# Kernel tuning notes

Hardware: AMD Instinct MI355X
Metric: run time of the kernel (lower is better)

Reference implementation:

```python
import jax, jax.numpy as jnp
import numpy as np

TEMPERATURE = 0.2
EPS = 1e-12

def _l2norm(x):
    # F.normalize(dim=1): x / max(||x||, eps)
    n = jnp.sqrt(jnp.sum(x * x, axis=1, keepdims=True))
    return x / jnp.maximum(n, EPS)

def setup_inputs() -> dict:
    key = jax.random.key(0)
    k1, k2, k3 = jax.random.split(key, 3)
    B, D, Q = 1024, 128, 65536
    return {
        "global_features_1": jax.random.normal(k1, (B, D), dtype=jnp.float32),
        "global_features_2": jax.random.normal(k2, (B, D), dtype=jnp.float32),
        "queue": jax.random.normal(k3, (Q, D), dtype=jnp.float32),
    }

def reference(global_features_1, global_features_2, queue):
    q = _l2norm(global_features_1)                    # [B, D]
    k = _l2norm(global_features_2)                    # [B, D]
    pos_sim = jnp.sum(q * k, axis=1, keepdims=True) / TEMPERATURE   # [B, 1]
    # queue renormalized under no_grad in the original
    queue_n = jax.lax.stop_gradient(_l2norm(queue))   # [Q, D]
    neg_sim = jnp.einsum('bd,qd->bq', q, queue_n) / TEMPERATURE     # [B, Q]
    logits = jnp.concatenate([pos_sim, neg_sim], axis=1)            # [B, 1+Q]
    # cross-entropy with label 0 for every row: -log_softmax(logits)[:, 0]
    log_probs = jax.nn.log_softmax(logits, axis=1)
    loss = -jnp.mean(log_probs[:, 0])
    return (loss, pos_sim, neg_sim)
```

## Files before the change

### kernel.cpp

```cpp
#include <hip/hip_runtime.h>
#include <math.h>

constexpr int B = 1024;
constexpr int D = 128;
constexpr int Q = 65536;
constexpr int NPART = 1024;
#define TEMP_INV 5.0f
#define EPS 1e-12f

typedef __bf16 bf16x8 __attribute__((ext_vector_type(8)));
typedef float  f32x4  __attribute__((ext_vector_type(4)));

__device__ __forceinline__ float wave_reduce_sum(float v) {
    #pragma unroll
    for (int off = 32; off > 0; off >>= 1) v += __shfl_xor(v, off);
    return v;
}

__device__ __forceinline__ unsigned short f2bf(float x) {
    unsigned int u = __float_as_uint(x);
    unsigned int r = (u + 0x7FFFu + ((u >> 16) & 1u)) >> 16;
    return (unsigned short)r;
}

__global__ void k_norm_pos(const float* __restrict__ g1,
                           const float* __restrict__ g2,
                           unsigned short* __restrict__ qnb,
                           float* __restrict__ out_pos,
                           float* __restrict__ ws_pos) {
    int b = blockIdx.x;
    int t = threadIdx.x;
    int w = t >> 6, lane = t & 63;
    float x = g1[b * D + t];
    float y = g2[b * D + t];
    __shared__ float sx[2], sy[2], sp[2];
    float xs = wave_reduce_sum(x * x);
    float ys = wave_reduce_sum(y * y);
    if (lane == 0) { sx[w] = xs; sy[w] = ys; }
    __syncthreads();
    float ix = 1.0f / fmaxf(sqrtf(sx[0] + sx[1]), EPS);
    float iy = 1.0f / fmaxf(sqrtf(sy[0] + sy[1]), EPS);
    float qv = x * ix;
    float kv = y * iy;
    qnb[b * D + t] = f2bf(qv);
    float p = wave_reduce_sum(qv * kv);
    if (lane == 0) sp[w] = p;
    __syncthreads();
    if (t == 0) {
        float pos = (sp[0] + sp[1]) * TEMP_INV;
        out_pos[b] = pos;
        ws_pos[b]  = pos;
    }
}

__global__ void k_qnorm(const float* __restrict__ queue,
                        unsigned short* __restrict__ qb) {
    int half = threadIdx.x >> 5;
    int l    = threadIdx.x & 31;
    int row  = blockIdx.x * 8 + half;
    float4 v = ((const float4*)(queue + (size_t)row * D))[l];
    float ss = v.x * v.x + v.y * v.y + v.z * v.z + v.w * v.w;
    #pragma unroll
    for (int off = 16; off > 0; off >>= 1) ss += __shfl_xor(ss, off);
    float inv = 1.0f / fmaxf(sqrtf(ss), EPS);
    uint2 o;
    o.x = (unsigned int)f2bf(v.x * inv) | ((unsigned int)f2bf(v.y * inv) << 16);
    o.y = (unsigned int)f2bf(v.z * inv) | ((unsigned int)f2bf(v.w * inv) << 16);
    ((uint2*)(qb + (size_t)row * D))[l] = o;
}

__global__ __launch_bounds__(256, 3) void k_gemm_mfma(const unsigned short* __restrict__ qnb,
                                                      const unsigned short* __restrict__ qb,
                                                      float* __restrict__ neg,
                                                      float* __restrict__ psum) {
    __shared__ unsigned short As[128][72];
    __shared__ unsigned short Bs[128][72];
    const int t  = threadIdx.x;
    const int bx = blockIdx.x;
    const int by = blockIdx.y;
    const int R0 = by * 128, C0 = bx * 128;
    const int wid = t >> 6, lane = t & 63;
    const int wr = wid >> 1, wc = wid & 1;
    const int lg = lane >> 4, lc = lane & 15;

    f32x4 acc[4][4];
    #pragma unroll
    for (int m = 0; m < 4; ++m)
        #pragma unroll
        for (int n = 0; n < 4; ++n)
            #pragma unroll
            for (int r = 0; r < 4; ++r) acc[m][n][r] = 0.0f;

    #pragma unroll
    for (int s = 0; s < 2; ++s) {
        if (s) __syncthreads();
        const int ks = s * 64;
        #pragma unroll
        for (int p = 0; p < 4; ++p) {
            int c   = t + 256 * p;
            int row = c >> 3;
            int off = (c & 7) * 8;
            uint4 va = *(const uint4*)(qnb + (size_t)(R0 + row) * D + ks + off);
            uint4 vb = *(const uint4*)(qb  + (size_t)(C0 + row) * D + ks + off);
            *(uint4*)&As[row][off] = va;
            *(uint4*)&Bs[row][off] = vb;
        }
        __syncthreads();
        #pragma unroll
        for (int kk = 0; kk < 64; kk += 32) {
            int ko = kk + lg * 8;
            bf16x8 a[4], b[4];
            #pragma unroll
            for (int m = 0; m < 4; ++m)
                a[m] = *(const bf16x8*)&As[wr * 64 + m * 16 + lc][ko];
            #pragma unroll
            for (int n = 0; n < 4; ++n)
                b[n] = *(const bf16x8*)&Bs[wc * 64 + n * 16 + lc][ko];
            #pragma unroll
            for (int m = 0; m < 4; ++m)
                #pragma unroll
                for (int n = 0; n < 4; ++n)
                    acc[m][n] = __builtin_amdgcn_mfma_f32_16x16x32_bf16(a[m], b[n], acc[m][n], 0, 0, 0);
        }
    }

    float* Cs = (float*)&Bs[0][0];
    const int slot = bx * 2 + wc;
    #pragma unroll
    for (int m = 0; m < 4; ++m) {
        __syncthreads();
        #pragma unroll
        for (int reg = 0; reg < 4; ++reg) {
            float v0 = acc[m][0][reg] * TEMP_INV;
            float v1 = acc[m][1][reg] * TEMP_INV;
            float v2 = acc[m][2][reg] * TEMP_INV;
            float v3 = acc[m][3][reg] * TEMP_INV;
            int cr = (wr * 16 + lg * 4 + reg) * 132 + wc * 64 + lc;
            Cs[cr +  0] = v0;
            Cs[cr + 16] = v1;
            Cs[cr + 32] = v2;
            Cs[cr + 48] = v3;
            float e = __expf(v0 - 5.0f) + __expf(v1 - 5.0f) +
                      __expf(v2 - 5.0f) + __expf(v3 - 5.0f);
            #pragma unroll
            for (int off = 1; off < 16; off <<= 1) e += __shfl_xor(e, off);
            if (lc == 0) {
                int gr = R0 + wr * 64 + m * 16 + lg * 4 + reg;
                psum[(size_t)gr * NPART + slot] = e;
            }
        }
        __syncthreads();
        #pragma unroll
        for (int p = 0; p < 4; ++p) {
            int f  = t + 256 * p;
            int lr = f >> 5, c4 = f & 31;
            int gr = R0 + (lr >> 4) * 64 + m * 16 + (lr & 15);
            float4 o = *(const float4*)&Cs[lr * 132 + c4 * 4];
            *(float4*)(neg + (size_t)gr * Q + C0 + c4 * 4) = o;
        }
    }
}

__global__ __launch_bounds__(256) void k_reduce_lse(const float* __restrict__ psum,
                                                    const float* __restrict__ ws_pos,
                                                    float* __restrict__ loss_b) {
    int r = blockIdx.x;
    const float4* pr = (const float4*)(psum + (size_t)r * NPART);
    float4 v = pr[threadIdx.x];
    float s = v.x + v.y + v.z + v.w;
    s = wave_reduce_sum(s);
    __shared__ float sw[4];
    int w = threadIdx.x >> 6, lane = threadIdx.x & 63;
    if (lane == 0) sw[w] = s;
    __syncthreads();
    if (threadIdx.x == 0) {
        float S = sw[0] + sw[1] + sw[2] + sw[3];
        float pos = ws_pos[r];
        S += __expf(pos - 5.0f);
        loss_b[r] = (logf(S) + 5.0f) - pos;
    }
}

__global__ void k_loss_mean(const float* __restrict__ loss_b, float* __restrict__ out) {
    float s = 0.0f;
    for (int i = threadIdx.x; i < B; i += 256) s += loss_b[i];
    s = wave_reduce_sum(s);
    __shared__ float sw[4];
    int w = threadIdx.x >> 6, lane = threadIdx.x & 63;
    if (lane == 0) sw[w] = s;
    __syncthreads();
    if (threadIdx.x == 0) out[0] = (sw[0] + sw[1] + sw[2] + sw[3]) / (float)B;
}

extern "C" void kernel_launch(void* const* d_in, const int* in_sizes, int n_in,
                              void* d_out, int out_size, void* d_ws, size_t ws_size,
                              hipStream_t stream) {
    const float* g1    = (const float*)d_in[0];
    const float* g2    = (const float*)d_in[1];
    const float* queue = (const float*)d_in[2];
    float* out = (float*)d_out;

    float* out_pos = out + 1;
    float* neg     = out + 1 + B;

    unsigned short* qnb = (unsigned short*)d_ws;
    unsigned short* qb  = qnb + (size_t)B * D;
    float* psum   = (float*)(qb + (size_t)Q * D);
    float* ws_pos = psum + (size_t)B * NPART;
    float* loss_b = ws_pos + B;

    k_norm_pos<<<B, 128, 0, stream>>>(g1, g2, qnb, out_pos, ws_pos);
    k_qnorm<<<Q / 8, 256, 0, stream>>>(queue, qb);
    dim3 g3(Q / 128, B / 128);
    k_gemm_mfma<<<g3, 256, 0, stream>>>(qnb, qb, neg, psum);
    k_reduce_lse<<<B, 256, 0, stream>>>(psum, ws_pos, loss_b);
    k_loss_mean<<<1, 256, 0, stream>>>(loss_b, out);
}
```

Measured before the change: 102.9 us.

## Merge prep kernels, use nontemporal loads/stores, raise GEMM occupancy hint

Merges the feature-normalization and queue-normalization kernels into one launch that branches on block index, removing one kernel launch. It adds nontemporal hints on the queue read and on the large neg-logit output writes, so these streaming accesses pollute the cache less. It also raises the GEMM launch-bounds occupancy hint from 3 to 4 blocks per SM, which may force register spilling.

```diff
diff --git a/kernel.cpp b/kernel.cpp
--- a/kernel.cpp
+++ b/kernel.cpp
@@ -23,53 +23,57 @@
     return (unsigned short)r;
 }
 
-__global__ void k_norm_pos(const float* __restrict__ g1,
-                           const float* __restrict__ g2,
-                           unsigned short* __restrict__ qnb,
-                           float* __restrict__ out_pos,
-                           float* __restrict__ ws_pos) {
-    int b = blockIdx.x;
-    int t = threadIdx.x;
-    int w = t >> 6, lane = t & 63;
-    float x = g1[b * D + t];
-    float y = g2[b * D + t];
-    __shared__ float sx[2], sy[2], sp[2];
-    float xs = wave_reduce_sum(x * x);
-    float ys = wave_reduce_sum(y * y);
-    if (lane == 0) { sx[w] = xs; sy[w] = ys; }
-    __syncthreads();
-    float ix = 1.0f / fmaxf(sqrtf(sx[0] + sx[1]), EPS);
-    float iy = 1.0f / fmaxf(sqrtf(sy[0] + sy[1]), EPS);
-    float qv = x * ix;
-    float kv = y * iy;
-    qnb[b * D + t] = f2bf(qv);
-    float p = wave_reduce_sum(qv * kv);
-    if (lane == 0) sp[w] = p;
-    __syncthreads();
-    if (t == 0) {
-        float pos = (sp[0] + sp[1]) * TEMP_INV;
-        out_pos[b] = pos;
-        ws_pos[b]  = pos;
-    }
-}
-
-__global__ void k_qnorm(const float* __restrict__ queue,
-                        unsigned short* __restrict__ qb) {
-    int half = threadIdx.x >> 5;
-    int l    = threadIdx.x & 31;
-    int row  = blockIdx.x * 8 + half;
-    float4 v = ((const float4*)(queue + (size_t)row * D))[l];
-    float ss = v.x * v.x + v.y * v.y + v.z * v.z + v.w * v.w;
-    #pragma unroll
-    for (int off = 16; off > 0; off >>= 1) ss += __shfl_xor(ss, off);
-    float inv = 1.0f / fmaxf(sqrtf(ss), EPS);
-    uint2 o;
-    o.x = (unsigned int)f2bf(v.x * inv) | ((unsigned int)f2bf(v.y * inv) << 16);
-    o.y = (unsigned int)f2bf(v.z * inv) | ((unsigned int)f2bf(v.w * inv) << 16);
-    ((uint2*)(qb + (size_t)row * D))[l] = o;
-}
-
-__global__ __launch_bounds__(256, 3) void k_gemm_mfma(const unsigned short* __restrict__ qnb,
+__global__ __launch_bounds__(256) void k_prep(const float* __restrict__ g1,
+                                              const float* __restrict__ g2,
+                                              const float* __restrict__ queue,
+                                              unsigned short* __restrict__ qnb,
+                                              unsigned short* __restrict__ qb,
+                                              float* __restrict__ out_pos,
+                                              float* __restrict__ ws_pos) {
+    if (blockIdx.x < Q / 8) {
+        int half = threadIdx.x >> 5;
+        int l    = threadIdx.x & 31;
+        int row  = blockIdx.x * 8 + half;
+        const f32x4* src = (const f32x4*)(queue + (size_t)row * D);
+        f32x4 v = __builtin_nontemporal_load(&src[l]);
+        float ss = v.x * v.x + v.y * v.y + v.z * v.z + v.w * v.w;
+        #pragma unroll
+        for (int off = 16; off > 0; off >>= 1) ss += __shfl_xor(ss, off);
+        float inv = 1.0f / fmaxf(sqrtf(ss), EPS);
+        uint2 o;
+        o.x = (unsigned int)f2bf(v.x * inv) | ((unsigned int)f2bf(v.y * inv) << 16);
+        o.y = (unsigned int)f2bf(v.z * inv) | ((unsigned int)f2bf(v.w * inv) << 16);
+        ((uint2*)(qb + (size_t)row * D))[l] = o;
+    } else {
+        int idx = blockIdx.x - Q / 8;
+        int w2 = threadIdx.x >> 7;
+        int tt = threadIdx.x & 127;
+        int b  = idx * 2 + w2;
+        int w  = tt >> 6, lane = tt & 63;
+        float x = g1[b * D + tt];
+        float y = g2[b * D + tt];
+        __shared__ float sx[2][2], sy[2][2], sp[2][2];
+        float xs = wave_reduce_sum(x * x);
+        float ys = wave_reduce_sum(y * y);
+        if (lane == 0) { sx[w2][w] = xs; sy[w2][w] = ys; }
+        __syncthreads();
+        float ix = 1.0f / fmaxf(sqrtf(sx[w2][0] + sx[w2][1]), EPS);
+        float iy = 1.0f / fmaxf(sqrtf(sy[w2][0] + sy[w2][1]), EPS);
+        float qv = x * ix;
+        float kv = y * iy;
+        qnb[b * D + tt] = f2bf(qv);
+        float p = wave_reduce_sum(qv * kv);
+        if (lane == 0) sp[w2][w] = p;
+        __syncthreads();
+        if (tt == 0) {
+            float pos = (sp[w2][0] + sp[w2][1]) * TEMP_INV;
+            out_pos[b] = pos;
+            ws_pos[b]  = pos;
+        }
+    }
+}
+
+__global__ __launch_bounds__(256, 4) void k_gemm_mfma(const unsigned short* __restrict__ qnb,
                                                       const unsigned short* __restrict__ qb,
                                                       float* __restrict__ neg,
                                                       float* __restrict__ psum) {
@@ -155,8 +159,8 @@
             int f  = t + 256 * p;
             int lr = f >> 5, c4 = f & 31;
             int gr = R0 + (lr >> 4) * 64 + m * 16 + (lr & 15);
-            float4 o = *(const float4*)&Cs[lr * 132 + c4 * 4];
-            *(float4*)(neg + (size_t)gr * Q + C0 + c4 * 4) = o;
+            f32x4 o = *(const f32x4*)&Cs[lr * 132 + c4 * 4];
+            __builtin_nontemporal_store(o, (f32x4*)(neg + (size_t)gr * Q + C0 + c4 * 4));
         }
     }
 }
@@ -209,8 +213,7 @@
     float* ws_pos = psum + (size_t)B * NPART;
     float* loss_b = ws_pos + B;
 
-    k_norm_pos<<<B, 128, 0, stream>>>(g1, g2, qnb, out_pos, ws_pos);
-    k_qnorm<<<Q / 8, 256, 0, stream>>>(queue, qb);
+    k_prep<<<Q / 8 + B / 2, 256, 0, stream>>>(g1, g2, queue, qnb, qb, out_pos, ws_pos);
     dim3 g3(Q / 128, B / 128);
     k_gemm_mfma<<<g3, 256, 0, stream>>>(qnb, qb, neg, psum);
     k_reduce_lse<<<B, 256, 0, stream>>>(psum, ws_pos, loss_b);
```

Result: slower. 117.4 us (+14.1%).
